# Performance work log

Hardware: AMD Instinct MI355X
Metric: run time of the kernel (lower is better)

The kernel has to match this reference:

```python
import jax, jax.numpy as jnp
import numpy as np

N, E, H, C, NG = 50000, 800000, 4, 64, 32
HC = H * C  # 256


def setup_inputs() -> dict:
    key = jax.random.key(0)
    ks = jax.random.split(key, 32)
    f32 = jnp.float32
    def rn(k, shape, s=0.1):
        return jax.random.normal(k, shape, dtype=f32) * s
    inp = {}
    inp['x'] = jax.random.normal(ks[0], (N, 4), dtype=f32)
    inp['edge_index'] = jax.random.randint(ks[1], (2, E), 0, N, dtype=jnp.int32)
    inp['edge_attr'] = jax.random.normal(ks[2], (E, 1), dtype=f32)
    inp['batch'] = jnp.sort(jax.random.randint(ks[3], (N,), 0, NG, dtype=jnp.int32))
    # encoder
    inp['enc_w'] = rn(ks[4], (4, 64)); inp['enc_b'] = rn(ks[5], (64,))
    # GATv2 layer 1: in 64 -> H*C (lin_l source, lin_r target, lin_edge, att, bias)
    inp['g1_wl'] = rn(ks[6], (64, HC)); inp['g1_bl'] = rn(ks[7], (HC,))
    inp['g1_wr'] = rn(ks[8], (64, HC)); inp['g1_br'] = rn(ks[9], (HC,))
    inp['g1_we'] = rn(ks[10], (1, HC))
    inp['g1_att'] = rn(ks[11], (H, C))
    inp['g1_bias'] = rn(ks[12], (HC,))
    # GATv2 layer 2: in 256 -> H*C
    inp['g2_wl'] = rn(ks[13], (HC, HC)); inp['g2_bl'] = rn(ks[14], (HC,))
    inp['g2_wr'] = rn(ks[15], (HC, HC)); inp['g2_br'] = rn(ks[16], (HC,))
    inp['g2_we'] = rn(ks[17], (1, HC))
    inp['g2_att'] = rn(ks[18], (H, C))
    inp['g2_bias'] = rn(ks[19], (HC,))
    # post MLP: 256 -> 128 (LayerNorm, ReLU) -> 64 (ReLU)
    inp['p1_w'] = rn(ks[20], (HC, 128)); inp['p1_b'] = rn(ks[21], (128,))
    inp['ln_g'] = jnp.ones((128,), dtype=f32); inp['ln_b'] = jnp.zeros((128,), dtype=f32)
    inp['p2_w'] = rn(ks[22], (128, 64)); inp['p2_b'] = rn(ks[23], (64,))
    return inp


def _gatv2_layer(x, src, dst, eattr, wl, bl, wr, br, we, att, bias):
    # PyG GATv2Conv: alpha_e = att . leaky_relu(lin_l(x_src) + lin_r(x_dst) + lin_edge(e))
    n = x.shape[0]
    xl = (x @ wl + bl).reshape(n, H, C)   # source-side messages
    xr = (x @ wr + br).reshape(n, H, C)   # target-side
    e = (eattr @ we).reshape(-1, H, C)
    m = jax.nn.leaky_relu(xl[src] + xr[dst] + e, 0.2)        # [E',H,C]
    alpha = jnp.einsum('ehc,hc->eh', m, att)                  # [E',H]
    amax = jax.lax.stop_gradient(jax.ops.segment_max(alpha, dst, num_segments=n))
    ex = jnp.exp(alpha - amax[dst])
    den = jax.ops.segment_sum(ex, dst, num_segments=n)
    a = ex / den[dst]                                          # softmax per dst node
    out = jax.ops.segment_sum(a[:, :, None] * xl[src], dst, num_segments=n)
    return out.reshape(n, HC) + bias


def reference(x, edge_index, edge_attr, batch, enc_w, enc_b,
              g1_wl, g1_bl, g1_wr, g1_br, g1_we, g1_att, g1_bias,
              g2_wl, g2_bl, g2_wr, g2_br, g2_we, g2_att, g2_bias,
              p1_w, p1_b, ln_g, ln_b, p2_w, p2_b):
    n = x.shape[0]
    src0, dst0 = edge_index[0], edge_index[1]
    # PyG default add_self_loops=True with fill_value='mean' for edge_attr
    deg = jnp.maximum(jax.ops.segment_sum(jnp.ones_like(edge_attr[:, 0]), dst0, num_segments=n), 1.0)
    loop_attr = jax.ops.segment_sum(edge_attr, dst0, num_segments=n) / deg[:, None]
    idx = jnp.arange(n, dtype=src0.dtype)
    src = jnp.concatenate([src0, idx]); dst = jnp.concatenate([dst0, idx])
    eattr = jnp.concatenate([edge_attr, loop_attr], axis=0)
    h = jax.nn.relu(x @ enc_w + enc_b)
    h = jax.nn.relu(_gatv2_layer(h, src, dst, eattr, g1_wl, g1_bl, g1_wr, g1_br, g1_we, g1_att, g1_bias))
    h = jax.nn.relu(_gatv2_layer(h, src, dst, eattr, g2_wl, g2_bl, g2_wr, g2_br, g2_we, g2_att, g2_bias))
    # global mean pool over graphs
    cnt = jnp.maximum(jax.ops.segment_sum(jnp.ones((n,), h.dtype), batch, num_segments=NG), 1.0)
    g = jax.ops.segment_sum(h, batch, num_segments=NG) / cnt[:, None]
    # post MLP (dropout is identity in eval)
    z = g @ p1_w + p1_b
    mu = jnp.mean(z, axis=-1, keepdims=True)
    var = jnp.mean((z - mu) ** 2, axis=-1, keepdims=True)
    z = (z - mu) / jnp.sqrt(var + 1e-5) * ln_g + ln_b
    z = jax.nn.relu(z)
    z = jax.nn.relu(z @ p2_w + p2_b)
    return z
```

## Files before the change

kernel.cpp:

```cpp
#include <hip/hip_runtime.h>

#define CDIV(a,b) (((a)+(b)-1)/(b))

typedef __bf16 bf16_t;
typedef unsigned char u8;
typedef bf16_t bf16x8 __attribute__((ext_vector_type(8)));
typedef float floatx4 __attribute__((ext_vector_type(4)));
typedef float floatx2 __attribute__((ext_vector_type(2)));

__device__ __forceinline__ int sigma2(int p) {
    int tile = p >> 7, hh = (p >> 6) & 1, m = (p >> 2) & 15, c = p & 3;
    return tile * 128 + (hh * 4 + c) * 16 + m;
}

__device__ __forceinline__ unsigned pack4_fp8(float a, float b, float c, float d) {
    int v = __builtin_amdgcn_cvt_pk_fp8_f32(a, b, 0, false);
    v = __builtin_amdgcn_cvt_pk_fp8_f32(c, d, v, true);
    return (unsigned)v;
}

template<bool HI>
__device__ __forceinline__ floatx2 cvtf8(unsigned v) {
    return __builtin_amdgcn_cvt_pk_f32_fp8(v, HI);
}

template<int CTRL>
__device__ __forceinline__ float dpp_add(float x) {
    int v = __builtin_amdgcn_update_dpp(0, __float_as_int(x), CTRL, 0xf, 0xf, true);
    return x + __int_as_float(v);
}

__global__ void k_deg(const int* __restrict__ ei, int* __restrict__ deg, int E) {
    int e = blockIdx.x * 256 + threadIdx.x;
    if (e >= E) return;
    atomicAdd(&deg[ei[E + e]], 1);
}

__global__ void k_scanA(const int* __restrict__ deg, int* __restrict__ part, int n) {
    __shared__ int sh[256];
    int t = threadIdx.x;
    int i = blockIdx.x * 256 + t;
    int v = (i < n) ? deg[i] + 1 : 0;
    sh[t] = v;
    __syncthreads();
    for (int d = 128; d > 0; d >>= 1) { if (t < d) sh[t] += sh[t + d]; __syncthreads(); }
    if (t == 0) part[blockIdx.x] = sh[0];
}
__global__ void k_scanB(int* __restrict__ part, int nb) {
    __shared__ int sh[256];
    int t = threadIdx.x;
    int v = (t < nb) ? part[t] : 0;
    sh[t] = v;
    __syncthreads();
    for (int d = 1; d < 256; d <<= 1) {
        int u = (t >= d) ? sh[t - d] : 0;
        __syncthreads();
        sh[t] += u;
        __syncthreads();
    }
    if (t < nb) part[t] = sh[t] - v;
}
__global__ void k_scanC(const int* __restrict__ deg, const int* __restrict__ part,
                        int* __restrict__ off, int n) {
    __shared__ int sh[256];
    int t = threadIdx.x;
    int i = blockIdx.x * 256 + t;
    int v = (i < n) ? deg[i] + 1 : 0;
    sh[t] = v;
    __syncthreads();
    for (int d = 1; d < 256; d <<= 1) {
        int u = (t >= d) ? sh[t - d] : 0;
        __syncthreads();
        sh[t] += u;
        __syncthreads();
    }
    int excl = part[blockIdx.x] + sh[t] - v;
    if (i < n) off[i] = excl;
    if (i == n - 1) off[n] = excl + v;
}

__global__ void k_fill(const int* __restrict__ ei, const float* __restrict__ ea,
                       const int* __restrict__ off, int* __restrict__ cursor,
                       int2* __restrict__ csr, int E) {
    int e = blockIdx.x * 256 + threadIdx.x;
    if (e >= E) return;
    int s = ei[e], d = ei[E + e];
    int pos = off[d] + atomicAdd(&cursor[d], 1);
    csr[pos] = make_int2(s, __float_as_int(ea[e]));
}

__global__ void k_selfloop(const int* __restrict__ off, int2* __restrict__ csr, int n) {
    int i = blockIdx.x * 256 + threadIdx.x;
    if (i >= n) return;
    int p0 = off[i], p1 = off[i + 1] - 1;
    float s = 0.0f;
    for (int p = p0; p < p1; ++p) s += __int_as_float(csr[p].y);
    float la = s / fmaxf((float)(p1 - p0), 1.0f);
    csr[p1] = make_int2(i, __float_as_int(la));
}

__global__ void k_wcast2(const float* __restrict__ Wl, const float* __restrict__ Wr,
                         const float* __restrict__ bl, const float* __restrict__ br,
                         bf16_t* __restrict__ Wt, float* __restrict__ bias2,
                         int K, int kshift, int permK,
                         const float* __restrict__ we, const float* __restrict__ att,
                         const float* __restrict__ cb,
                         float* __restrict__ wep, float* __restrict__ attp,
                         float* __restrict__ cbp) {
    int idx = blockIdx.x * 256 + threadIdx.x;
    if (idx < 512) bias2[idx] = (idx < 256) ? bl[idx] : br[idx - 256];
    if (idx < 256) {
        int sg = sigma2(idx);
        wep[idx] = we[sg]; attp[idx] = att[sg]; cbp[idx] = cb[sg];
    }
    if (idx >= 512 * K) return;
    int nn = idx >> kshift, k = idx & (K - 1);
    int ks = permK ? sigma2(k) : k;
    float v = (nn < 256) ? Wl[ks * 256 + nn] : Wr[ks * 256 + (nn - 256)];
    Wt[idx] = (bf16_t)v;
}

__global__ __launch_bounds__(256) void k_gemm1_fused(
        const float* __restrict__ x, const float* __restrict__ encw,
        const float* __restrict__ encb, const bf16_t* __restrict__ Wt,
        const float* __restrict__ bias2, u8* __restrict__ XL,
        u8* __restrict__ XR, int nrows) {
    __shared__ bf16_t As[128 * 32];
    __shared__ bf16_t Bs[128 * 32];
    int tid = threadIdx.x;
    int w = tid >> 6, lane = tid & 63;
    int quad = lane >> 4, m = lane & 15;
    int row0 = blockIdx.x * 128;
    int ct0 = blockIdx.y * 2;
    bf16x8 afr[2][2];
    floatx4 acc[2][8];

    for (int ctile = ct0; ctile < ct0 + 2; ++ctile) {
        int n0 = ctile * 128;
#pragma unroll
        for (int rt = 0; rt < 2; ++rt)
#pragma unroll
            for (int ct = 0; ct < 8; ++ct)
                acc[rt][ct] = (floatx4){0.f, 0.f, 0.f, 0.f};
        for (int k0c = 0; k0c < 2; ++k0c) {
            __syncthreads();
            if (ctile == ct0) {
#pragma unroll
                for (int i = 0; i < 2; ++i) {
                    int c = tid + i * 256;
                    int r = c >> 2, kc = c & 3;
                    int sw = (kc + (r >> 1)) & 3;
                    int gr = row0 + r; if (gr >= nrows) gr = nrows - 1;
                    float4 xv = ((const float4*)x)[gr];
                    bf16x8 v;
#pragma unroll
                    for (int kk = 0; kk < 8; ++kk) {
                        int k = k0c * 32 + kc * 8 + kk;
                        float s = encb[k];
                        s = fmaf(xv.x, encw[k], s);
                        s = fmaf(xv.y, encw[64 + k], s);
                        s = fmaf(xv.z, encw[128 + k], s);
                        s = fmaf(xv.w, encw[192 + k], s);
                        v[kk] = (bf16_t)fmaxf(s, 0.0f);
                    }
                    *(bf16x8*)&As[r * 32 + sw * 8] = v;
                }
            }
#pragma unroll
            for (int i = 0; i < 2; ++i) {
                int c = tid + i * 256;
                int r = c >> 2, kc = c & 3;
                int sw = (kc + (r >> 1)) & 3;
                bf16x8 v = *(const bf16x8*)&Wt[(size_t)(n0 + r) * 64 + k0c * 32 + kc * 8];
                *(bf16x8*)&Bs[r * 32 + sw * 8] = v;
            }
            __syncthreads();
            if (ctile == ct0) {
#pragma unroll
                for (int rt = 0; rt < 2; ++rt) {
                    int ar = w * 32 + rt * 16 + m;
                    afr[k0c][rt] = *(bf16x8*)&As[ar * 32 + (((quad + (ar >> 1)) & 3) * 8)];
                }
            }
            bf16x8 bfr[8];
#pragma unroll
            for (int ct = 0; ct < 8; ++ct) {
                int br = ct * 16 + m;
                bfr[ct] = *(bf16x8*)&Bs[br * 32 + (((quad + (br >> 1)) & 3) * 8)];
            }
#pragma unroll
            for (int ct = 0; ct < 8; ++ct) {
                acc[0][ct] = __builtin_amdgcn_mfma_f32_16x16x32_bf16(afr[k0c][0], bfr[ct], acc[0][ct], 0, 0, 0);
                acc[1][ct] = __builtin_amdgcn_mfma_f32_16x16x32_bf16(afr[k0c][1], bfr[ct], acc[1][ct], 0, 0, 0);
            }
        }
        int tile = ctile & 1;
        u8* dst = (ctile < 2) ? XL : XR;
        float bv[8];
#pragma unroll
        for (int ct = 0; ct < 8; ++ct) bv[ct] = bias2[n0 + ct * 16 + m];
#pragma unroll
        for (int rt = 0; rt < 2; ++rt) {
#pragma unroll
            for (int i = 0; i < 4; ++i) {
                int row = row0 + w * 32 + rt * 16 + quad * 4 + i;
                if (row < nrows) {
                    unsigned w0 = pack4_fp8(acc[rt][0][i] + bv[0], acc[rt][1][i] + bv[1],
                                            acc[rt][2][i] + bv[2], acc[rt][3][i] + bv[3]);
                    unsigned w1 = pack4_fp8(acc[rt][4][i] + bv[4], acc[rt][5][i] + bv[5],
                                            acc[rt][6][i] + bv[6], acc[rt][7][i] + bv[7]);
                    *(unsigned*)&dst[(size_t)row * 256 + tile * 128 + m * 4] = w0;
                    *(unsigned*)&dst[(size_t)row * 256 + tile * 128 + 64 + m * 4] = w1;
                }
            }
        }
    }
}

__global__ __launch_bounds__(256) void k_gemm2(
        const bf16_t* __restrict__ Hb, const bf16_t* __restrict__ Wt,
        const float* __restrict__ bias2, u8* __restrict__ XL,
        u8* __restrict__ XR, int nrows) {
    const int K = 256;
    __shared__ bf16_t As[128 * 32];
    __shared__ bf16_t Bs[128 * 32];
    int tid = threadIdx.x;
    int w = tid >> 6, lane = tid & 63;
    int quad = lane >> 4, m = lane & 15;
    int row0 = blockIdx.x * 128;
    int ct0 = blockIdx.y * 2;
    bf16x8 afr[8][2];
    floatx4 acc[2][8];

    for (int ctile = ct0; ctile < ct0 + 2; ++ctile) {
        int n0 = ctile * 128;
#pragma unroll
        for (int rt = 0; rt < 2; ++rt)
#pragma unroll
            for (int ct = 0; ct < 8; ++ct)
                acc[rt][ct] = (floatx4){0.f, 0.f, 0.f, 0.f};
        for (int k0c = 0; k0c < 8; ++k0c) {
            __syncthreads();
            if (ctile == ct0) {
#pragma unroll
                for (int i = 0; i < 2; ++i) {
                    int c = tid + i * 256;
                    int r = c >> 2, kc = c & 3;
                    int sw = (kc + (r >> 1)) & 3;
                    int gr = row0 + r; if (gr >= nrows) gr = nrows - 1;
                    bf16x8 v = *(const bf16x8*)&Hb[(size_t)gr * K + k0c * 32 + kc * 8];
                    *(bf16x8*)&As[r * 32 + sw * 8] = v;
                }
            }
#pragma unroll
            for (int i = 0; i < 2; ++i) {
                int c = tid + i * 256;
                int r = c >> 2, kc = c & 3;
                int sw = (kc + (r >> 1)) & 3;
                bf16x8 v = *(const bf16x8*)&Wt[(size_t)(n0 + r) * K + k0c * 32 + kc * 8];
                *(bf16x8*)&Bs[r * 32 + sw * 8] = v;
            }
            __syncthreads();
            if (ctile == ct0) {
#pragma unroll
                for (int rt = 0; rt < 2; ++rt) {
                    int ar = w * 32 + rt * 16 + m;
                    afr[k0c][rt] = *(bf16x8*)&As[ar * 32 + (((quad + (ar >> 1)) & 3) * 8)];
                }
            }
            bf16x8 bfr[8];
#pragma unroll
            for (int ct = 0; ct < 8; ++ct) {
                int br = ct * 16 + m;
                bfr[ct] = *(bf16x8*)&Bs[br * 32 + (((quad + (br >> 1)) & 3) * 8)];
            }
#pragma unroll
            for (int ct = 0; ct < 8; ++ct) {
                acc[0][ct] = __builtin_amdgcn_mfma_f32_16x16x32_bf16(afr[k0c][0], bfr[ct], acc[0][ct], 0, 0, 0);
                acc[1][ct] = __builtin_amdgcn_mfma_f32_16x16x32_bf16(afr[k0c][1], bfr[ct], acc[1][ct], 0, 0, 0);
            }
        }
        int tile = ctile & 1;
        u8* dst = (ctile < 2) ? XL : XR;
        float bv[8];
#pragma unroll
        for (int ct = 0; ct < 8; ++ct) bv[ct] = bias2[n0 + ct * 16 + m];
#pragma unroll
        for (int rt = 0; rt < 2; ++rt) {
#pragma unroll
            for (int i = 0; i < 4; ++i) {
                int row = row0 + w * 32 + rt * 16 + quad * 4 + i;
                if (row < nrows) {
                    unsigned w0 = pack4_fp8(acc[rt][0][i] + bv[0], acc[rt][1][i] + bv[1],
                                            acc[rt][2][i] + bv[2], acc[rt][3][i] + bv[3]);
                    unsigned w1 = pack4_fp8(acc[rt][4][i] + bv[4], acc[rt][5][i] + bv[5],
                                            acc[rt][6][i] + bv[6], acc[rt][7][i] + bv[7]);
                    *(unsigned*)&dst[(size_t)row * 256 + tile * 128 + m * 4] = w0;
                    *(unsigned*)&dst[(size_t)row * 256 + tile * 128 + 64 + m * 4] = w1;
                }
            }
        }
    }
}

__global__ void k_conv(
                       const u8* __restrict__ XL, const u8* __restrict__ XR,
                       const float* __restrict__ wep, const float* __restrict__ attp,
                       const int2* __restrict__ csr,
                       const int* __restrict__ off, const float* __restrict__ cbp,
                       bf16_t* __restrict__ outb, int n) {
    int wid = (blockIdx.x * 256 + threadIdx.x) >> 6;
    int lane = threadIdx.x & 63;
    if (wid >= n) return;
    int l = lane & 31, half = lane >> 5;
    int loff = l * 8;
    uint2 ur = *(const uint2*)(XR + (size_t)wid * 256 + loff);
    floatx2 xr01 = cvtf8<false>(ur.x);
    floatx2 xr23 = cvtf8<true>(ur.x);
    floatx2 xr45 = cvtf8<false>(ur.y);
    floatx2 xr67 = cvtf8<true>(ur.y);
    float4 wa = ((const float4*)wep)[2 * l], wb = ((const float4*)wep)[2 * l + 1];
    float4 aa = ((const float4*)attp)[2 * l], ab = ((const float4*)attp)[2 * l + 1];
    floatx2 wv01 = {wa.x, wa.y}, wv23 = {wa.z, wa.w};
    floatx2 wv45 = {wb.x, wb.y}, wv67 = {wb.z, wb.w};
    const float LOG2E = 1.44269504f;
    floatx2 av01 = {aa.x * LOG2E, aa.y * LOG2E}, av23 = {aa.z * LOG2E, aa.w * LOG2E};
    floatx2 av45 = {ab.x * LOG2E, ab.y * LOG2E}, av67 = {ab.z * LOG2E, ab.w * LOG2E};
    int p0 = off[wid], p1 = off[wid + 1];
    float s = 0.f;
    floatx2 a01 = {0.f, 0.f}, a23 = {0.f, 0.f}, a45 = {0.f, 0.f}, a67 = {0.f, 0.f};

    for (int base = p0; base < p1; base += 64) {
        int rem = p1 - base;
        int cnt = (rem < 64) ? rem : 64;
        int gp = base + lane; if (gp > p1 - 1) gp = p1 - 1;
        int2 ed = csr[gp];

        auto fetch = [&](int j, uint2& u, float& ev) {
            int sl = j + half; if (sl >= cnt) sl = cnt - 1;
            int sx = __shfl(ed.x, sl);
            ev = __int_as_float(__shfl(ed.y, sl));
            u = *(const uint2*)(XL + (size_t)sx * 256 + loff);
        };

        uint2 u0, u1, u2; float e0, e1, e2;
        fetch(0, u0, e0);
        fetch(2, u1, e1);
        fetch(4, u2, e2);

#pragma unroll 3
        for (int j = 0; j < cnt; j += 2) {
            uint2 un; float en;
            fetch(j + 6, un, en);
            floatx2 x01 = cvtf8<false>(u0.x);
            floatx2 x23 = cvtf8<true>(u0.x);
            floatx2 x45 = cvtf8<false>(u0.y);
            floatx2 x67 = cvtf8<true>(u0.y);
            floatx2 t01 = x01 + xr01 + e0 * wv01;
            floatx2 t23 = x23 + xr23 + e0 * wv23;
            floatx2 t45 = x45 + xr45 + e0 * wv45;
            floatx2 t67 = x67 + xr67 + e0 * wv67;
            t01 = __builtin_elementwise_max(t01, 0.2f * t01);
            t23 = __builtin_elementwise_max(t23, 0.2f * t23);
            t45 = __builtin_elementwise_max(t45, 0.2f * t45);
            t67 = __builtin_elementwise_max(t67, 0.2f * t67);
            floatx2 d = t01 * av01 + t23 * av23 + t45 * av45 + t67 * av67;
            float al = d.x + d.y;
            al = dpp_add<0xB1>(al);
            al = dpp_add<0x4E>(al);
            al = dpp_add<0x141>(al);
            float wg = (j + half < cnt) ? exp2f(al) : 0.0f;
            s += wg;
            a01 += wg * x01; a23 += wg * x23; a45 += wg * x45; a67 += wg * x67;
            u0 = u1; e0 = e1; u1 = u2; e1 = e2; u2 = un; e2 = en;
        }
    }

    s += __shfl_xor(s, 32);
    a01.x += __shfl_xor(a01.x, 32); a01.y += __shfl_xor(a01.y, 32);
    a23.x += __shfl_xor(a23.x, 32); a23.y += __shfl_xor(a23.y, 32);
    a45.x += __shfl_xor(a45.x, 32); a45.y += __shfl_xor(a45.y, 32);
    a67.x += __shfl_xor(a67.x, 32); a67.y += __shfl_xor(a67.y, 32);
    if (half == 0) {
        float inv = 1.0f / s;
        float4 ba = ((const float4*)cbp)[2 * l], bb = ((const float4*)cbp)[2 * l + 1];
        bf16x8 ob;
        ob[0] = (bf16_t)fmaxf(fmaf(a01.x, inv, ba.x), 0.f);
        ob[1] = (bf16_t)fmaxf(fmaf(a01.y, inv, ba.y), 0.f);
        ob[2] = (bf16_t)fmaxf(fmaf(a23.x, inv, ba.z), 0.f);
        ob[3] = (bf16_t)fmaxf(fmaf(a23.y, inv, ba.w), 0.f);
        ob[4] = (bf16_t)fmaxf(fmaf(a45.x, inv, bb.x), 0.f);
        ob[5] = (bf16_t)fmaxf(fmaf(a45.y, inv, bb.y), 0.f);
        ob[6] = (bf16_t)fmaxf(fmaf(a67.x, inv, bb.z), 0.f);
        ob[7] = (bf16_t)fmaxf(fmaf(a67.y, inv, bb.w), 0.f);
        *(bf16x8*)&outb[(size_t)wid * 256 + l * 8] = ob;
    }
}

__global__ void k_pool(const bf16_t* __restrict__ h, const int* __restrict__ batch,
                       float* __restrict__ gsum, float* __restrict__ gcnt, int n) {
    int j = threadIdx.x;
    int start = blockIdx.x * 32;
    if (start >= n) return;
    int end = start + 32; if (end > n) end = n;
    int cur = batch[start];
    float acc = 0.0f, cnt = 0.0f;
    for (int i = start; i < end; ++i) {
        int g = batch[i];
        if (g != cur) {
            atomicAdd(&gsum[cur * 256 + j], acc);
            if (j == 0) atomicAdd(&gcnt[cur], cnt);
            acc = 0.0f; cnt = 0.0f; cur = g;
        }
        acc += (float)h[(size_t)i * 256 + j];
        cnt += 1.0f;
    }
    atomicAdd(&gsum[cur * 256 + j], acc);
    if (j == 0) atomicAdd(&gcnt[cur], cnt);
}

__global__ void k_mlp(const float* __restrict__ gsum, const float* __restrict__ gcnt,
                      const float* __restrict__ p1w, const float* __restrict__ p1b,
                      const float* __restrict__ lng, const float* __restrict__ lnb,
                      const float* __restrict__ p2w, const float* __restrict__ p2b,
                      float* __restrict__ out) {
    int g = blockIdx.x;
    int t = threadIdx.x;
    __shared__ float gv[256];
    __shared__ float z[128];
    __shared__ float red[128];
    float invc = 1.0f / fmaxf(gcnt[g], 1.0f);
    gv[sigma2(t)]       = gsum[g * 256 + t] * invc;
    gv[sigma2(t + 128)] = gsum[g * 256 + 128 + t] * invc;
    __syncthreads();
    float z1 = p1b[t];
    for (int k = 0; k < 256; ++k) z1 = fmaf(gv[k], p1w[k * 128 + t], z1);
    red[t] = z1;
    __syncthreads();
    for (int d = 64; d > 0; d >>= 1) { if (t < d) red[t] += red[t + d]; __syncthreads(); }
    float mu = red[0] * (1.0f / 128.0f);
    __syncthreads();
    float dz = z1 - mu;
    red[t] = dz * dz;
    __syncthreads();
    for (int d = 64; d > 0; d >>= 1) { if (t < d) red[t] += red[t + d]; __syncthreads(); }
    float var = red[0] * (1.0f / 128.0f);
    float zn = dz * rsqrtf(var + 1e-5f) * lng[t] + lnb[t];
    z[t] = fmaxf(zn, 0.0f);
    __syncthreads();
    if (t < 64) {
        float o = p2b[t];
        for (int k = 0; k < 128; ++k) o = fmaf(z[k], p2w[k * 64 + t], o);
        out[g * 64 + t] = fmaxf(o, 0.0f);
    }
}

extern "C" void kernel_launch(void* const* d_in, const int* in_sizes, int n_in,
                              void* d_out, int out_size, void* d_ws, size_t ws_size,
                              hipStream_t stream) {
    const float* x      = (const float*)d_in[0];
    const int*   ei     = (const int*)d_in[1];
    const float* ea     = (const float*)d_in[2];
    const int*   batch  = (const int*)d_in[3];
    const float* enc_w  = (const float*)d_in[4];
    const float* enc_b  = (const float*)d_in[5];
    const float* g1_wl  = (const float*)d_in[6];
    const float* g1_bl  = (const float*)d_in[7];
    const float* g1_wr  = (const float*)d_in[8];
    const float* g1_br  = (const float*)d_in[9];
    const float* g1_we  = (const float*)d_in[10];
    const float* g1_att = (const float*)d_in[11];
    const float* g1_bias= (const float*)d_in[12];
    const float* g2_wl  = (const float*)d_in[13];
    const float* g2_bl  = (const float*)d_in[14];
    const float* g2_wr  = (const float*)d_in[15];
    const float* g2_br  = (const float*)d_in[16];
    const float* g2_we  = (const float*)d_in[17];
    const float* g2_att = (const float*)d_in[18];
    const float* g2_bias= (const float*)d_in[19];
    const float* p1_w   = (const float*)d_in[20];
    const float* p1_b   = (const float*)d_in[21];
    const float* ln_g   = (const float*)d_in[22];
    const float* ln_b   = (const float*)d_in[23];
    const float* p2_w   = (const float*)d_in[24];
    const float* p2_b   = (const float*)d_in[25];
    float* out = (float*)d_out;

    const int N  = in_sizes[3];
    const int E  = in_sizes[1] / 2;
    const int EE = E + N;
    const int NB = CDIV(N, 256);

    u8*     XL  = (u8*)d_ws;
    u8*     XR  = XL + (size_t)N * 256;
    bf16_t* Hb  = (bf16_t*)(XR + (size_t)N * 256);
    bf16_t* Wt  = Hb + (size_t)N * 256;
    int2*  csr  = (int2*)(Wt + 512 * 256);
    float* gsum  = (float*)(csr + EE);
    float* gcnt  = gsum + 32 * 256;
    int*   deg   = (int*)(gcnt + 32);
    int*   cursor= deg + N;
    float* bias2 = (float*)(cursor + N);
    float* wep   = bias2 + 512;
    float* attp  = wep + 256;
    float* cbp   = attp + 256;
    int*   part  = (int*)(cbp + 256);
    int*   off   = part + 256;

    (void)hipMemsetAsync(gsum, 0, (size_t)(2 * N + 32 * 256 + 32) * sizeof(float), stream);

    k_deg<<<CDIV(E, 256), 256, 0, stream>>>(ei, deg, E);
    k_scanA<<<NB, 256, 0, stream>>>(deg, part, N);
    k_scanB<<<1, 256, 0, stream>>>(part, NB);
    k_scanC<<<NB, 256, 0, stream>>>(deg, part, off, N);
    k_fill<<<CDIV(E, 256), 256, 0, stream>>>(ei, ea, off, cursor, csr, E);
    k_selfloop<<<NB, 256, 0, stream>>>(off, csr, N);

    dim3 ggrid(CDIV(N, 128), 2);

    k_wcast2<<<CDIV(512 * 64, 256), 256, 0, stream>>>(g1_wl, g1_wr, g1_bl, g1_br, Wt, bias2,
                                                      64, 6, 0, g1_we, g1_att, g1_bias,
                                                      wep, attp, cbp);
    k_gemm1_fused<<<ggrid, 256, 0, stream>>>(x, enc_w, enc_b, Wt, bias2, XL, XR, N);
    k_conv<<<CDIV(N, 4), 256, 0, stream>>>(XL, XR, wep, attp, csr, off, cbp, Hb, N);

    k_wcast2<<<CDIV(512 * 256, 256), 256, 0, stream>>>(g2_wl, g2_wr, g2_bl, g2_br, Wt, bias2,
                                                       256, 8, 1, g2_we, g2_att, g2_bias,
                                                       wep, attp, cbp);
    k_gemm2<<<ggrid, 256, 0, stream>>>(Hb, Wt, bias2, XL, XR, N);
    k_conv<<<CDIV(N, 4), 256, 0, stream>>>(XL, XR, wep, attp, csr, off, cbp, Hb, N);

    k_pool<<<CDIV(N, 32), 256, 0, stream>>>(Hb, batch, gsum, gcnt, N);
    k_mlp<<<32, 128, 0, stream>>>(gsum, gcnt, p1_w, p1_b, ln_g, ln_b, p2_w, p2_b, out);
}
```

Measured before the change: 425.3 us.

## Process four edges per wavefront with 16-byte fp8 loads in GATv2 conv

The conv kernel now splits each 64-lane wavefront into four 16-lane groups, each handling one edge with 16-byte fp8 gathers, so four edges are processed per iteration instead of two. Leaky-ReLU is rewritten as 0.6*t + 0.4*|t| with the constants folded into the attention vector. The per-head reduction needs one fewer DPP step. The cost is more registers per lane (16 channels held instead of 8), which may reduce occupancy, plus an extra cross-group shuffle reduction at the end.

```diff
diff --git a/kernel.cpp b/kernel.cpp
--- a/kernel.cpp
+++ b/kernel.cpp
@@ -312,23 +312,34 @@
     int wid = (blockIdx.x * 256 + threadIdx.x) >> 6;
     int lane = threadIdx.x & 63;
     if (wid >= n) return;
-    int l = lane & 31, half = lane >> 5;
-    int loff = l * 8;
-    uint2 ur = *(const uint2*)(XR + (size_t)wid * 256 + loff);
-    floatx2 xr01 = cvtf8<false>(ur.x);
-    floatx2 xr23 = cvtf8<true>(ur.x);
-    floatx2 xr45 = cvtf8<false>(ur.y);
-    floatx2 xr67 = cvtf8<true>(ur.y);
-    float4 wa = ((const float4*)wep)[2 * l], wb = ((const float4*)wep)[2 * l + 1];
-    float4 aa = ((const float4*)attp)[2 * l], ab = ((const float4*)attp)[2 * l + 1];
-    floatx2 wv01 = {wa.x, wa.y}, wv23 = {wa.z, wa.w};
-    floatx2 wv45 = {wb.x, wb.y}, wv67 = {wb.z, wb.w};
-    const float LOG2E = 1.44269504f;
-    floatx2 av01 = {aa.x * LOG2E, aa.y * LOG2E}, av23 = {aa.z * LOG2E, aa.w * LOG2E};
-    floatx2 av45 = {ab.x * LOG2E, ab.y * LOG2E}, av67 = {ab.z * LOG2E, ab.w * LOG2E};
+    int g = lane >> 4;
+    int li = lane & 15;
+    int loff = li * 16;
+
+    uint4 ur = *(const uint4*)(XR + (size_t)wid * 256 + loff);
+    floatx2 xr[8];
+    xr[0] = cvtf8<false>(ur.x); xr[1] = cvtf8<true>(ur.x);
+    xr[2] = cvtf8<false>(ur.y); xr[3] = cvtf8<true>(ur.y);
+    xr[4] = cvtf8<false>(ur.z); xr[5] = cvtf8<true>(ur.z);
+    xr[6] = cvtf8<false>(ur.w); xr[7] = cvtf8<true>(ur.w);
+
+    floatx2 wv[8], av6[8];
+    const float C6 = 0.6f * 1.44269504f;
+#pragma unroll
+    for (int q = 0; q < 4; ++q) {
+        float4 wq = ((const float4*)wep)[4 * li + q];
+        float4 aq = ((const float4*)attp)[4 * li + q];
+        wv[2 * q]     = (floatx2){wq.x, wq.y};
+        wv[2 * q + 1] = (floatx2){wq.z, wq.w};
+        av6[2 * q]     = (floatx2){aq.x * C6, aq.y * C6};
+        av6[2 * q + 1] = (floatx2){aq.z * C6, aq.w * C6};
+    }
+
     int p0 = off[wid], p1 = off[wid + 1];
     float s = 0.f;
-    floatx2 a01 = {0.f, 0.f}, a23 = {0.f, 0.f}, a45 = {0.f, 0.f}, a67 = {0.f, 0.f};
+    floatx2 a[8];
+#pragma unroll
+    for (int q = 0; q < 8; ++q) a[q] = (floatx2){0.f, 0.f};
 
     for (int base = p0; base < p1; base += 64) {
         int rem = p1 - base;
@@ -336,64 +347,78 @@
         int gp = base + lane; if (gp > p1 - 1) gp = p1 - 1;
         int2 ed = csr[gp];
 
-        auto fetch = [&](int j, uint2& u, float& ev) {
-            int sl = j + half; if (sl >= cnt) sl = cnt - 1;
+        auto fetch = [&](int j, uint4& u, float& ev) {
+            int sl = j + g; if (sl >= cnt) sl = cnt - 1;
             int sx = __shfl(ed.x, sl);
             ev = __int_as_float(__shfl(ed.y, sl));
-            u = *(const uint2*)(XL + (size_t)sx * 256 + loff);
+            u = *(const uint4*)(XL + (unsigned)sx * 256u + (unsigned)loff);
         };
 
-        uint2 u0, u1, u2; float e0, e1, e2;
+        uint4 u0, u1, u2; float e0, e1, e2;
         fetch(0, u0, e0);
-        fetch(2, u1, e1);
-        fetch(4, u2, e2);
+        fetch(4, u1, e1);
+        fetch(8, u2, e2);
 
 #pragma unroll 3
-        for (int j = 0; j < cnt; j += 2) {
-            uint2 un; float en;
-            fetch(j + 6, un, en);
-            floatx2 x01 = cvtf8<false>(u0.x);
-            floatx2 x23 = cvtf8<true>(u0.x);
-            floatx2 x45 = cvtf8<false>(u0.y);
-            floatx2 x67 = cvtf8<true>(u0.y);
-            floatx2 t01 = x01 + xr01 + e0 * wv01;
-            floatx2 t23 = x23 + xr23 + e0 * wv23;
-            floatx2 t45 = x45 + xr45 + e0 * wv45;
-            floatx2 t67 = x67 + xr67 + e0 * wv67;
-            t01 = __builtin_elementwise_max(t01, 0.2f * t01);
-            t23 = __builtin_elementwise_max(t23, 0.2f * t23);
-            t45 = __builtin_elementwise_max(t45, 0.2f * t45);
-            t67 = __builtin_elementwise_max(t67, 0.2f * t67);
-            floatx2 d = t01 * av01 + t23 * av23 + t45 * av45 + t67 * av67;
-            float al = d.x + d.y;
+        for (int j = 0; j < cnt; j += 4) {
+            uint4 un; float en;
+            fetch(j + 12, un, en);
+            floatx2 x[8];
+            x[0] = cvtf8<false>(u0.x); x[1] = cvtf8<true>(u0.x);
+            x[2] = cvtf8<false>(u0.y); x[3] = cvtf8<true>(u0.y);
+            x[4] = cvtf8<false>(u0.z); x[5] = cvtf8<true>(u0.z);
+            x[6] = cvtf8<false>(u0.w); x[7] = cvtf8<true>(u0.w);
+            floatx2 d6, db;
+            {
+                floatx2 t = x[0] + xr[0] + e0 * wv[0];
+                d6 = av6[0] * t;
+                db.x = av6[0].x * fabsf(t.x);
+                db.y = av6[0].y * fabsf(t.y);
+            }
+#pragma unroll
+            for (int q = 1; q < 8; ++q) {
+                floatx2 t = x[q] + xr[q] + e0 * wv[q];
+                d6 += av6[q] * t;
+                db.x = fmaf(av6[q].x, fabsf(t.x), db.x);
+                db.y = fmaf(av6[q].y, fabsf(t.y), db.y);
+            }
+            float al = fmaf(0.66666667f, db.x + db.y, d6.x + d6.y);
             al = dpp_add<0xB1>(al);
             al = dpp_add<0x4E>(al);
-            al = dpp_add<0x141>(al);
-            float wg = (j + half < cnt) ? exp2f(al) : 0.0f;
+            float wg = (j + g < cnt) ? exp2f(al) : 0.0f;
             s += wg;
-            a01 += wg * x01; a23 += wg * x23; a45 += wg * x45; a67 += wg * x67;
+#pragma unroll
+            for (int q = 0; q < 8; ++q) a[q] += wg * x[q];
             u0 = u1; e0 = e1; u1 = u2; e1 = e2; u2 = un; e2 = en;
         }
     }
 
+    s += __shfl_xor(s, 16);
     s += __shfl_xor(s, 32);
-    a01.x += __shfl_xor(a01.x, 32); a01.y += __shfl_xor(a01.y, 32);
-    a23.x += __shfl_xor(a23.x, 32); a23.y += __shfl_xor(a23.y, 32);
-    a45.x += __shfl_xor(a45.x, 32); a45.y += __shfl_xor(a45.y, 32);
-    a67.x += __shfl_xor(a67.x, 32); a67.y += __shfl_xor(a67.y, 32);
-    if (half == 0) {
+#pragma unroll
+    for (int q = 0; q < 8; ++q) {
+        a[q].x += __shfl_xor(a[q].x, 16); a[q].y += __shfl_xor(a[q].y, 16);
+        a[q].x += __shfl_xor(a[q].x, 32); a[q].y += __shfl_xor(a[q].y, 32);
+    }
+    if (g == 0) {
         float inv = 1.0f / s;
-        float4 ba = ((const float4*)cbp)[2 * l], bb = ((const float4*)cbp)[2 * l + 1];
-        bf16x8 ob;
-        ob[0] = (bf16_t)fmaxf(fmaf(a01.x, inv, ba.x), 0.f);
-        ob[1] = (bf16_t)fmaxf(fmaf(a01.y, inv, ba.y), 0.f);
-        ob[2] = (bf16_t)fmaxf(fmaf(a23.x, inv, ba.z), 0.f);
-        ob[3] = (bf16_t)fmaxf(fmaf(a23.y, inv, ba.w), 0.f);
-        ob[4] = (bf16_t)fmaxf(fmaf(a45.x, inv, bb.x), 0.f);
-        ob[5] = (bf16_t)fmaxf(fmaf(a45.y, inv, bb.y), 0.f);
-        ob[6] = (bf16_t)fmaxf(fmaf(a67.x, inv, bb.z), 0.f);
-        ob[7] = (bf16_t)fmaxf(fmaf(a67.y, inv, bb.w), 0.f);
-        *(bf16x8*)&outb[(size_t)wid * 256 + l * 8] = ob;
+        float cb[16];
+#pragma unroll
+        for (int q = 0; q < 4; ++q) {
+            float4 bq = ((const float4*)cbp)[4 * li + q];
+            cb[4 * q] = bq.x; cb[4 * q + 1] = bq.y;
+            cb[4 * q + 2] = bq.z; cb[4 * q + 3] = bq.w;
+        }
+        bf16x8 o0, o1;
+#pragma unroll
+        for (int q = 0; q < 4; ++q) {
+            o0[2 * q]     = (bf16_t)fmaxf(fmaf(a[q].x, inv, cb[2 * q]), 0.f);
+            o0[2 * q + 1] = (bf16_t)fmaxf(fmaf(a[q].y, inv, cb[2 * q + 1]), 0.f);
+            o1[2 * q]     = (bf16_t)fmaxf(fmaf(a[q + 4].x, inv, cb[8 + 2 * q]), 0.f);
+            o1[2 * q + 1] = (bf16_t)fmaxf(fmaf(a[q + 4].y, inv, cb[8 + 2 * q + 1]), 0.f);
+        }
+        *(bf16x8*)&outb[(size_t)wid * 256 + loff] = o0;
+        *(bf16x8*)&outb[(size_t)wid * 256 + loff + 8] = o1;
     }
 }
 
```

Result: slower. 460.1 us (+8.2%).

## Split each node's edge aggregation across two wavefronts with shared-memory merge

Applied to the files above, without the earlier changes.

The GATv2 aggregation kernel now assigns two wavefronts per destination node instead of one. Edges are interleaved between the waves in pairs, and the partial softmax sums and weighted accumulators are combined through shared memory after a block barrier. This halves the serial per-wave edge loop and doubles the number of waves in flight, which should help hide gather latency. The cost is extra waves, a __syncthreads, and a redundant XR load per node. The gather address also switches to 32-bit unsigned arithmetic.

```diff
diff --git a/kernel.cpp b/kernel.cpp
--- a/kernel.cpp
+++ b/kernel.cpp
@@ -309,12 +309,18 @@
                        const int2* __restrict__ csr,
                        const int* __restrict__ off, const float* __restrict__ cbp,
                        bf16_t* __restrict__ outb, int n) {
-    int wid = (blockIdx.x * 256 + threadIdx.x) >> 6;
-    int lane = threadIdx.x & 63;
-    if (wid >= n) return;
-    int l = lane & 31, half = lane >> 5;
+    int tid = threadIdx.x;
+    int w = tid >> 6;
+    int nib = w >> 1;
+    int hs = w & 1;
+    int node = blockIdx.x * 2 + nib;
+    int lane = tid & 63;
+    int half = lane >> 5, l = lane & 31;
     int loff = l * 8;
-    uint2 ur = *(const uint2*)(XR + (size_t)wid * 256 + loff);
+    bool active = node < n;
+    int nc = active ? node : n - 1;
+
+    uint2 ur = *(const uint2*)(XR + (size_t)nc * 256 + loff);
     floatx2 xr01 = cvtf8<false>(ur.x);
     floatx2 xr23 = cvtf8<true>(ur.x);
     floatx2 xr45 = cvtf8<false>(ur.y);
@@ -326,53 +332,58 @@
     const float LOG2E = 1.44269504f;
     floatx2 av01 = {aa.x * LOG2E, aa.y * LOG2E}, av23 = {aa.z * LOG2E, aa.w * LOG2E};
     floatx2 av45 = {ab.x * LOG2E, ab.y * LOG2E}, av67 = {ab.z * LOG2E, ab.w * LOG2E};
-    int p0 = off[wid], p1 = off[wid + 1];
+    int p0 = off[nc], p1 = off[nc + 1];
     float s = 0.f;
     floatx2 a01 = {0.f, 0.f}, a23 = {0.f, 0.f}, a45 = {0.f, 0.f}, a67 = {0.f, 0.f};
 
-    for (int base = p0; base < p1; base += 64) {
-        int rem = p1 - base;
-        int cnt = (rem < 64) ? rem : 64;
-        int gp = base + lane; if (gp > p1 - 1) gp = p1 - 1;
-        int2 ed = csr[gp];
-
-        auto fetch = [&](int j, uint2& u, float& ev) {
-            int sl = j + half; if (sl >= cnt) sl = cnt - 1;
-            int sx = __shfl(ed.x, sl);
-            ev = __int_as_float(__shfl(ed.y, sl));
-            u = *(const uint2*)(XL + (size_t)sx * 256 + loff);
-        };
-
-        uint2 u0, u1, u2; float e0, e1, e2;
-        fetch(0, u0, e0);
-        fetch(2, u1, e1);
-        fetch(4, u2, e2);
+    if (active) {
+        for (int cbase = p0; cbase < p1; cbase += 128) {
+            int gp = cbase + 2 * hs + ((lane >> 1) << 2) + (lane & 1);
+            bool vld = gp < p1;
+            int gpc = vld ? gp : p1 - 1;
+            int2 ed = csr[gpc];
+            int cnt = (int)__popcll(__ballot(vld));
+
+            if (cnt > 0) {
+                auto fetch = [&](int j, uint2& u, float& ev) {
+                    int sl = j + half; if (sl >= cnt) sl = cnt - 1;
+                    int sx = __shfl(ed.x, sl);
+                    ev = __int_as_float(__shfl(ed.y, sl));
+                    u = *(const uint2*)(XL + (unsigned)(sx * 256 + loff));
+                };
+
+                uint2 u0, u1, u2; float e0, e1, e2;
+                fetch(0, u0, e0);
+                fetch(2, u1, e1);
+                fetch(4, u2, e2);
 
 #pragma unroll 3
-        for (int j = 0; j < cnt; j += 2) {
-            uint2 un; float en;
-            fetch(j + 6, un, en);
-            floatx2 x01 = cvtf8<false>(u0.x);
-            floatx2 x23 = cvtf8<true>(u0.x);
-            floatx2 x45 = cvtf8<false>(u0.y);
-            floatx2 x67 = cvtf8<true>(u0.y);
-            floatx2 t01 = x01 + xr01 + e0 * wv01;
-            floatx2 t23 = x23 + xr23 + e0 * wv23;
-            floatx2 t45 = x45 + xr45 + e0 * wv45;
-            floatx2 t67 = x67 + xr67 + e0 * wv67;
-            t01 = __builtin_elementwise_max(t01, 0.2f * t01);
-            t23 = __builtin_elementwise_max(t23, 0.2f * t23);
-            t45 = __builtin_elementwise_max(t45, 0.2f * t45);
-            t67 = __builtin_elementwise_max(t67, 0.2f * t67);
-            floatx2 d = t01 * av01 + t23 * av23 + t45 * av45 + t67 * av67;
-            float al = d.x + d.y;
-            al = dpp_add<0xB1>(al);
-            al = dpp_add<0x4E>(al);
-            al = dpp_add<0x141>(al);
-            float wg = (j + half < cnt) ? exp2f(al) : 0.0f;
-            s += wg;
-            a01 += wg * x01; a23 += wg * x23; a45 += wg * x45; a67 += wg * x67;
-            u0 = u1; e0 = e1; u1 = u2; e1 = e2; u2 = un; e2 = en;
+                for (int j = 0; j < cnt; j += 2) {
+                    uint2 un; float en;
+                    fetch(j + 6, un, en);
+                    floatx2 x01 = cvtf8<false>(u0.x);
+                    floatx2 x23 = cvtf8<true>(u0.x);
+                    floatx2 x45 = cvtf8<false>(u0.y);
+                    floatx2 x67 = cvtf8<true>(u0.y);
+                    floatx2 t01 = x01 + xr01 + e0 * wv01;
+                    floatx2 t23 = x23 + xr23 + e0 * wv23;
+                    floatx2 t45 = x45 + xr45 + e0 * wv45;
+                    floatx2 t67 = x67 + xr67 + e0 * wv67;
+                    t01 = __builtin_elementwise_max(t01, 0.2f * t01);
+                    t23 = __builtin_elementwise_max(t23, 0.2f * t23);
+                    t45 = __builtin_elementwise_max(t45, 0.2f * t45);
+                    t67 = __builtin_elementwise_max(t67, 0.2f * t67);
+                    floatx2 d = t01 * av01 + t23 * av23 + t45 * av45 + t67 * av67;
+                    float al = d.x + d.y;
+                    al = dpp_add<0xB1>(al);
+                    al = dpp_add<0x4E>(al);
+                    al = dpp_add<0x141>(al);
+                    float wg = (j + half < cnt) ? exp2f(al) : 0.0f;
+                    s += wg;
+                    a01 += wg * x01; a23 += wg * x23; a45 += wg * x45; a67 += wg * x67;
+                    u0 = u1; e0 = e1; u1 = u2; e1 = e2; u2 = un; e2 = en;
+                }
+            }
         }
     }
 
@@ -381,7 +392,20 @@
     a23.x += __shfl_xor(a23.x, 32); a23.y += __shfl_xor(a23.y, 32);
     a45.x += __shfl_xor(a45.x, 32); a45.y += __shfl_xor(a45.y, 32);
     a67.x += __shfl_xor(a67.x, 32); a67.y += __shfl_xor(a67.y, 32);
-    if (half == 0) {
+
+    __shared__ float shm[2][32][9];
+    if (active && hs == 1 && half == 0) {
+        float* d = shm[nib][l];
+        d[0] = s;
+        d[1] = a01.x; d[2] = a01.y; d[3] = a23.x; d[4] = a23.y;
+        d[5] = a45.x; d[6] = a45.y; d[7] = a67.x; d[8] = a67.y;
+    }
+    __syncthreads();
+    if (active && hs == 0 && half == 0) {
+        const float* m = shm[nib][l];
+        s += m[0];
+        a01.x += m[1]; a01.y += m[2]; a23.x += m[3]; a23.y += m[4];
+        a45.x += m[5]; a45.y += m[6]; a67.x += m[7]; a67.y += m[8];
         float inv = 1.0f / s;
         float4 ba = ((const float4*)cbp)[2 * l], bb = ((const float4*)cbp)[2 * l + 1];
         bf16x8 ob;
@@ -393,7 +417,7 @@
         ob[5] = (bf16_t)fmaxf(fmaf(a45.y, inv, bb.y), 0.f);
         ob[6] = (bf16_t)fmaxf(fmaf(a67.x, inv, bb.z), 0.f);
         ob[7] = (bf16_t)fmaxf(fmaf(a67.y, inv, bb.w), 0.f);
-        *(bf16x8*)&outb[(size_t)wid * 256 + l * 8] = ob;
+        *(bf16x8*)&outb[(size_t)node * 256 + l * 8] = ob;
     }
 }
 
@@ -522,13 +546,13 @@
                                                       64, 6, 0, g1_we, g1_att, g1_bias,
                                                       wep, attp, cbp);
     k_gemm1_fused<<<ggrid, 256, 0, stream>>>(x, enc_w, enc_b, Wt, bias2, XL, XR, N);
-    k_conv<<<CDIV(N, 4), 256, 0, stream>>>(XL, XR, wep, attp, csr, off, cbp, Hb, N);
+    k_conv<<<CDIV(N, 2), 256, 0, stream>>>(XL, XR, wep, attp, csr, off, cbp, Hb, N);
 
     k_wcast2<<<CDIV(512 * 256, 256), 256, 0, stream>>>(g2_wl, g2_wr, g2_bl, g2_br, Wt, bias2,
                                                        256, 8, 1, g2_we, g2_att, g2_bias,
                                                        wep, attp, cbp);
     k_gemm2<<<ggrid, 256, 0, stream>>>(Hb, Wt, bias2, XL, XR, N);
-    k_conv<<<CDIV(N, 4), 256, 0, stream>>>(XL, XR, wep, attp, csr, off, cbp, Hb, N);
+    k_conv<<<CDIV(N, 2), 256, 0, stream>>>(XL, XR, wep, attp, csr, off, cbp, Hb, N);
 
     k_pool<<<CDIV(N, 32), 256, 0, stream>>>(Hb, batch, gsum, gcnt, N);
     k_mlp<<<32, 128, 0, stream>>>(gsum, gcnt, p1_w, p1_b, ln_g, ln_b, p2_w, p2_b, out);
```

New measurement: 444.5 us. 1.05x slower.

## Process conv nodes in descending-degree order via a degree-bucket permutation

Applied to the files above, without the earlier changes.

Builds a counting-sort permutation of nodes by in-degree, highest first, using three small kernels (histogram, 64-bin scan, scatter). Both conv launches then map each wavefront to perm[wid], so heavy nodes start early and the tail of long-running waves gets shorter. It also narrows the XL gather address arithmetic to 32 bits. The cost is three extra launches and a memset, plus scattered XR, offset and output accesses that are no longer coalesced across adjacent waves.

```diff
diff --git a/kernel.cpp b/kernel.cpp
--- a/kernel.cpp
+++ b/kernel.cpp
@@ -34,6 +34,32 @@
     int e = blockIdx.x * 256 + threadIdx.x;
     if (e >= E) return;
     atomicAdd(&deg[ei[E + e]], 1);
+}
+
+__global__ void k_hist(const int* __restrict__ deg, int* __restrict__ hcnt, int n) {
+    int i = blockIdx.x * 256 + threadIdx.x;
+    if (i >= n) return;
+    int d = deg[i]; if (d > 63) d = 63;
+    atomicAdd(&hcnt[63 - d], 1);
+}
+__global__ void k_hscan(const int* __restrict__ hcnt, int* __restrict__ hoff) {
+    int t = threadIdx.x;
+    int v = hcnt[t];
+    int s = v;
+    for (int d = 1; d < 64; d <<= 1) {
+        int u = __shfl_up(s, d);
+        if (t >= d) s += u;
+    }
+    hoff[t] = s - v;
+}
+__global__ void k_scatter(const int* __restrict__ deg, const int* __restrict__ hoff,
+                          int* __restrict__ hcur, int* __restrict__ perm, int n) {
+    int i = blockIdx.x * 256 + threadIdx.x;
+    if (i >= n) return;
+    int d = deg[i]; if (d > 63) d = 63;
+    int b = 63 - d;
+    int pos = hoff[b] + atomicAdd(&hcur[b], 1);
+    perm[pos] = i;
 }
 
 __global__ void k_scanA(const int* __restrict__ deg, int* __restrict__ part, int n) {
@@ -308,13 +334,15 @@
                        const float* __restrict__ wep, const float* __restrict__ attp,
                        const int2* __restrict__ csr,
                        const int* __restrict__ off, const float* __restrict__ cbp,
+                       const int* __restrict__ perm,
                        bf16_t* __restrict__ outb, int n) {
     int wid = (blockIdx.x * 256 + threadIdx.x) >> 6;
     int lane = threadIdx.x & 63;
     if (wid >= n) return;
+    int node = perm[wid];
     int l = lane & 31, half = lane >> 5;
     int loff = l * 8;
-    uint2 ur = *(const uint2*)(XR + (size_t)wid * 256 + loff);
+    uint2 ur = *(const uint2*)(XR + (size_t)node * 256 + loff);
     floatx2 xr01 = cvtf8<false>(ur.x);
     floatx2 xr23 = cvtf8<true>(ur.x);
     floatx2 xr45 = cvtf8<false>(ur.y);
@@ -326,7 +354,7 @@
     const float LOG2E = 1.44269504f;
     floatx2 av01 = {aa.x * LOG2E, aa.y * LOG2E}, av23 = {aa.z * LOG2E, aa.w * LOG2E};
     floatx2 av45 = {ab.x * LOG2E, ab.y * LOG2E}, av67 = {ab.z * LOG2E, ab.w * LOG2E};
-    int p0 = off[wid], p1 = off[wid + 1];
+    int p0 = off[node], p1 = off[node + 1];
     float s = 0.f;
     floatx2 a01 = {0.f, 0.f}, a23 = {0.f, 0.f}, a45 = {0.f, 0.f}, a67 = {0.f, 0.f};
 
@@ -340,7 +368,7 @@
             int sl = j + half; if (sl >= cnt) sl = cnt - 1;
             int sx = __shfl(ed.x, sl);
             ev = __int_as_float(__shfl(ed.y, sl));
-            u = *(const uint2*)(XL + (size_t)sx * 256 + loff);
+            u = *(const uint2*)(XL + (unsigned)(sx * 256 + loff));
         };
 
         uint2 u0, u1, u2; float e0, e1, e2;
@@ -393,7 +421,7 @@
         ob[5] = (bf16_t)fmaxf(fmaf(a45.y, inv, bb.y), 0.f);
         ob[6] = (bf16_t)fmaxf(fmaf(a67.x, inv, bb.z), 0.f);
         ob[7] = (bf16_t)fmaxf(fmaf(a67.y, inv, bb.w), 0.f);
-        *(bf16x8*)&outb[(size_t)wid * 256 + l * 8] = ob;
+        *(bf16x8*)&outb[(size_t)node * 256 + l * 8] = ob;
     }
 }
 
@@ -506,10 +534,19 @@
     float* cbp   = attp + 256;
     int*   part  = (int*)(cbp + 256);
     int*   off   = part + 256;
+    int*   perm  = off + (N + 1);
+    int*   hcnt  = perm + N;
+    int*   hcur  = hcnt + 64;
+    int*   hoff  = hcur + 64;
 
     (void)hipMemsetAsync(gsum, 0, (size_t)(2 * N + 32 * 256 + 32) * sizeof(float), stream);
+    (void)hipMemsetAsync(hcnt, 0, 128 * sizeof(int), stream);
 
     k_deg<<<CDIV(E, 256), 256, 0, stream>>>(ei, deg, E);
+    k_hist<<<NB, 256, 0, stream>>>(deg, hcnt, N);
+    k_hscan<<<1, 64, 0, stream>>>(hcnt, hoff);
+    k_scatter<<<NB, 256, 0, stream>>>(deg, hoff, hcur, perm, N);
+
     k_scanA<<<NB, 256, 0, stream>>>(deg, part, N);
     k_scanB<<<1, 256, 0, stream>>>(part, NB);
     k_scanC<<<NB, 256, 0, stream>>>(deg, part, off, N);
@@ -522,13 +559,13 @@
                                                       64, 6, 0, g1_we, g1_att, g1_bias,
                                                       wep, attp, cbp);
     k_gemm1_fused<<<ggrid, 256, 0, stream>>>(x, enc_w, enc_b, Wt, bias2, XL, XR, N);
-    k_conv<<<CDIV(N, 4), 256, 0, stream>>>(XL, XR, wep, attp, csr, off, cbp, Hb, N);
+    k_conv<<<CDIV(N, 4), 256, 0, stream>>>(XL, XR, wep, attp, csr, off, cbp, perm, Hb, N);
 
     k_wcast2<<<CDIV(512 * 256, 256), 256, 0, stream>>>(g2_wl, g2_wr, g2_bl, g2_br, Wt, bias2,
                                                        256, 8, 1, g2_we, g2_att, g2_bias,
                                                        wep, attp, cbp);
     k_gemm2<<<ggrid, 256, 0, stream>>>(Hb, Wt, bias2, XL, XR, N);
-    k_conv<<<CDIV(N, 4), 256, 0, stream>>>(XL, XR, wep, attp, csr, off, cbp, Hb, N);
+    k_conv<<<CDIV(N, 4), 256, 0, stream>>>(XL, XR, wep, attp, csr, off, cbp, perm, Hb, N);
 
     k_pool<<<CDIV(N, 32), 256, 0, stream>>>(Hb, batch, gsum, gcnt, N);
     k_mlp<<<32, 128, 0, stream>>>(gsum, gcnt, p1_w, p1_b, ln_g, ln_b, p2_w, p2_b, out);
```

Measured after the change: 693.0 us. +63.0%, slower.
